# Kernel tuning notes

Hardware: AMD Instinct MI355X
Metric: run time of the kernel (lower is better)

## Reference

```python
import jax, jax.numpy as jnp
import numpy as np
import math

T, R, H, DK = 3, 4, 8, 32   # num_types, num_relations, n_heads, d_k
OUT = H * DK                # out_dim = 256
IN = 256                    # in_dim (== out_dim, required by residual)
B, N = 4, 1024              # batch, max_nodes
LN_EPS = 1e-5


def setup_inputs() -> dict:
    key = jax.random.key(0)
    ks = jax.random.split(key, 12)
    a = math.sqrt(6.0 / (2 * DK))  # xavier_uniform bound for [d_k,d_k]
    w = 0.02
    return {
        "node_features":   jax.random.normal(ks[0], (B, N, IN), jnp.float32),
        "node_types_soft": jax.random.uniform(ks[1], (B, N, T), jnp.float32),
        "adj_matrix_soft": jax.random.uniform(ks[2], (B, N, N), jnp.float32),
        "edge_types_soft": jax.random.uniform(ks[3], (B, N, N, R), jnp.float32),
        "Wq": jax.random.normal(ks[4], (T, IN, OUT), jnp.float32) * w,
        "bq": jnp.zeros((T, OUT), jnp.float32),
        "Wk": jax.random.normal(ks[5], (T, IN, OUT), jnp.float32) * w,
        "bk": jnp.zeros((T, OUT), jnp.float32),
        "Wv": jax.random.normal(ks[6], (T, IN, OUT), jnp.float32) * w,
        "bv": jnp.zeros((T, OUT), jnp.float32),
        "Wa": jax.random.normal(ks[7], (T, OUT, OUT), jnp.float32) * w,
        "ba": jnp.zeros((T, OUT), jnp.float32),
        "rel_pri": jnp.ones((R, H), jnp.float32),
        "rel_att": jax.random.uniform(ks[8], (R, H, DK, DK), jnp.float32, -a, a),
        "rel_msg": jax.random.uniform(ks[9], (R, H, DK, DK), jnp.float32, -a, a),
        "skip": jnp.ones((T,), jnp.float32),
        "ln_gamma": jnp.ones((T, OUT), jnp.float32),
        "ln_beta": jnp.zeros((T, OUT), jnp.float32),
    }


def _single(x, types, adj, erel, Wq, bq, Wk, bk, Wv, bv, Wa, ba,
            rel_pri, rel_att, rel_msg, skip, ln_gamma, ln_beta):
    # x:[N,in], types:[N,T], adj:[N,N], erel:[N,N,R]
    n = x.shape[0]
    sqrt_dk = float(np.sqrt(DK))
    # per-type projections -> [T,N,H,DK]
    Qt = (jnp.einsum('nd,tdo->tno', x, Wq) + bq[:, None, :]).reshape(T, n, H, DK)
    Kt = (jnp.einsum('nd,tdo->tno', x, Wk) + bk[:, None, :]).reshape(T, n, H, DK)
    Vt = (jnp.einsum('nd,tdo->tno', x, Wv) + bv[:, None, :]).reshape(T, n, H, DK)
    # relation-transformed K/V: [T,R,N,H,DK]
    Ksr = jnp.einsum('tnhd,rhde->trnhe', Kt, rel_att)
    Vsr = jnp.einsum('tnhd,rhde->trnhe', Vt, rel_msg)
    # soft-type mixtures (sums over target/source types factor out of the mask)
    Qbar = jnp.einsum('nt,tnhd->nhd', types, Qt)            # target mix
    Kbar = jnp.einsum('nt,trnhd->rnhd', types, Ksr)         # source mix, per relation
    # accumulated (masked, unnormalized) attention logits [N,N,H]
    res_att = jnp.zeros((n, n, H), x.dtype)
    for r in range(R):
        coef = (adj * erel[:, :, r])[:, :, None] * (rel_pri[r] / sqrt_dk)  # [N,N,H]
        res_att = res_att + coef * jnp.einsum('ihd,jhd->ijh', Qbar, Kbar[r])
    # per-target-row softmax over sources (dim j), zeroed if row-sum tiny
    row_sum = res_att.sum(axis=(1, 2))                       # [N]
    attn = jnp.where((row_sum > 1e-6)[:, None, None],
                     jax.nn.softmax(res_att, axis=1), 0.0)
    # aggregated = sum_{s,r,j} attn * masked score * V_{s,r}  (never builds [N,N,H,DK])
    agg = jnp.zeros((n, H, DK), x.dtype)
    for r in range(R):
        coef = (adj * erel[:, :, r])[:, :, None] * (rel_pri[r] / sqrt_dk)
        for s in range(T):
            score = coef * types[None, :, s, None] * jnp.einsum('ihd,jhd->ijh', Qbar, Ksr[s, r])
            agg = agg + jnp.einsum('ijh,ijh,jhd->ihd', attn, score, Vsr[s, r])
    agg = agg.reshape(n, OUT)
    # per-type output head: a_linear(gelu(agg)), gated residual, layernorm, soft-type mix
    g = jax.nn.gelu(agg, approximate=False)
    trans = jnp.einsum('no,tod->tnd', g, Wa) + ba[:, None, :]          # [T,N,OUT]
    alpha = jax.nn.sigmoid(skip)[:, None, None]
    res = trans * alpha + x[None] * (1.0 - alpha)
    mu = res.mean(axis=-1, keepdims=True)
    var = ((res - mu) ** 2).mean(axis=-1, keepdims=True)
    ln = (res - mu) / jnp.sqrt(var + LN_EPS) * ln_gamma[:, None, :] + ln_beta[:, None, :]
    return jnp.einsum('nt,tnd->nd', types, ln)


def reference(node_features, node_types_soft, adj_matrix_soft, edge_types_soft,
              Wq, bq, Wk, bk, Wv, bv, Wa, ba, rel_pri, rel_att, rel_msg,
              skip, ln_gamma, ln_beta):
    f = jax.vmap(_single, in_axes=(0, 0, 0, 0) + (None,) * 14)
    return f(node_features, node_types_soft, adj_matrix_soft, edge_types_soft,
             Wq, bq, Wk, bk, Wv, bv, Wa, ba, rel_pri, rel_att, rel_msg,
             skip, ln_gamma, ln_beta)
```

## Files before the change

### kernel.cpp

```cpp
#include <hip/hip_runtime.h>
#include <math.h>

constexpr int CB = 4, CN = 1024, CT = 3, CR = 4, CH = 8, CDK = 32, COUT = 256;

typedef __attribute__((ext_vector_type(4))) float f32x4;
typedef __attribute__((ext_vector_type(8))) short s16x8;
typedef __attribute__((ext_vector_type(2))) _Float16 f16x2;
typedef __attribute__((ext_vector_type(4))) _Float16 f16x4;
typedef __attribute__((ext_vector_type(8))) _Float16 f16x8;
typedef __attribute__((ext_vector_type(4))) unsigned short u16x4;
typedef __attribute__((ext_vector_type(8))) unsigned short u16x8;

union W4 { f16x4 v4; f16x2 v2[2]; };

__device__ inline unsigned short f2bf(float x) {
    unsigned u = __float_as_uint(x);
    unsigned r = (u + 0x7fffu + ((u >> 16) & 1u)) >> 16;
    return (unsigned short)r;
}
__device__ inline float bf2f(unsigned short b) {
    return __uint_as_float(((unsigned)b) << 16);
}
__device__ inline f16x2 pk2(float a, float b) {
    auto t = __builtin_amdgcn_cvt_pkrtz(a, b);
    f16x2 r;
    __builtin_memcpy(&r, &t, sizeof(r));
    return r;
}

__global__ __launch_bounds__(256) void prep0(
    const float* __restrict__ nf,
    unsigned short* __restrict__ Xh, unsigned short* __restrict__ Xl,
    const float* __restrict__ Wq, const float* __restrict__ Wk,
    const float* __restrict__ Wv, const float* __restrict__ Wa,
    unsigned short* __restrict__ WTh, unsigned short* __restrict__ WTl,
    const float* __restrict__ rel_msg, _Float16* __restrict__ MT,
    float* __restrict__ rs,
    const float* __restrict__ adj, const float* __restrict__ erel,
    float* __restrict__ coefT)
{
    __shared__ float smem[32 * 132];
    const int bx = blockIdx.x, tid = threadIdx.x;
    if (bx < 1024) {
        size_t idx = ((size_t)bx * 256 + tid) * 4;
        f32x4 v = *(const f32x4*)(nf + idx);
        u16x4 hv, lv;
        #pragma unroll
        for (int k = 0; k < 4; ++k) {
            unsigned short hb = f2bf(v[k]);
            hv[k] = hb; lv[k] = f2bf(v[k] - bf2f(hb));
        }
        *(u16x4*)(Xh + idx) = hv;
        *(u16x4*)(Xl + idx) = lv;
    } else if (bx < 1792) {
        int w = bx - 1024;
        int zz = w >> 6; int rem = w & 63;
        int k0 = (rem >> 3) * 32, n0 = (rem & 7) * 32;
        int t = zz % 3;
        const float* W;
        if (zz < 9) { int w3 = zz / 3; W = (w3 == 0 ? Wq : (w3 == 1 ? Wk : Wv)); }
        else W = Wa;
        W += (size_t)t * COUT * COUT;
        {
            int k = tid >> 3, n4 = (tid & 7) * 4;
            f32x4 v = *(const f32x4*)(W + (size_t)(k0 + k) * COUT + n0 + n4);
            smem[(n4 + 0) * 33 + k] = v[0]; smem[(n4 + 1) * 33 + k] = v[1];
            smem[(n4 + 2) * 33 + k] = v[2]; smem[(n4 + 3) * 33 + k] = v[3];
        }
        __syncthreads();
        int n = tid >> 3, k4 = (tid & 7) * 4;
        u16x4 hv, lv;
        #pragma unroll
        for (int j = 0; j < 4; ++j) {
            float x = smem[n * 33 + k4 + j];
            unsigned short hb = f2bf(x);
            hv[j] = hb; lv[j] = f2bf(x - bf2f(hb));
        }
        size_t off = (size_t)zz * COUT * COUT + (size_t)(n0 + n) * COUT + k0 + k4;
        *(u16x4*)(WTh + off) = hv;
        *(u16x4*)(WTl + off) = lv;
    } else if (bx < 1824) {
        int rh = bx - 1792;
        int e = tid >> 3, ep4 = (tid & 7) * 4;
        f16x4 o;
        #pragma unroll
        for (int k = 0; k < 4; ++k)
            o[k] = (_Float16)rel_msg[((size_t)rh * 32 + ep4 + k) * 32 + e];
        *(f16x4*)(MT + ((size_t)rh * 32 + e) * 32 + ep4) = o;
    } else if (bx < 1840) {
        rs[(bx - 1824) * 256 + tid] = 0.f;
    } else {
        int c = bx - 1840;
        int b = c >> 10; int rem = c & 1023;
        int i0 = (rem >> 5) * 32; int j0 = (rem & 31) * 32;
        {
            int ii = tid >> 3, jc = tid & 7;
            size_t arow = ((size_t)b * CN + i0 + ii) * CN + j0;
            f32x4 av = *(const f32x4*)(adj + arow + jc * 4);
            #pragma unroll
            for (int kk = 0; kk < 4; ++kk) {
                int j = jc * 4 + kk;
                f32x4 ev = *(const f32x4*)(erel + (arow + j) * 4);
                float a = av[kk];
                f32x4 cv;
                cv[0] = ev[0] * a; cv[1] = ev[1] * a; cv[2] = ev[2] * a; cv[3] = ev[3] * a;
                *(f32x4*)&smem[j * 132 + ii * 4] = cv;
            }
        }
        __syncthreads();
        {
            int jj = tid >> 3, ic = tid & 7;
            size_t orow = ((size_t)b * CN + j0 + jj) * CN + i0;
            #pragma unroll
            for (int kk = 0; kk < 4; ++kk)
                *(f32x4*)(coefT + (orow + ic * 4 + kk) * 4) =
                    *(const f32x4*)&smem[jj * 132 + (ic * 4 + kk) * 4];
        }
    }
}

__global__ __launch_bounds__(256) void mfma_gemm(
    int mode,
    const unsigned short* __restrict__ Ah, const unsigned short* __restrict__ Al,
    const unsigned short* __restrict__ WTh, const unsigned short* __restrict__ WTl,
    const float* __restrict__ bq, const float* __restrict__ bk,
    const float* __restrict__ bv, const float* __restrict__ ba,
    float* __restrict__ Y0, float* __restrict__ Y1, float* __restrict__ Y2)
{
    int z = blockIdx.z;
    int b, t, widx;
    const float* bias;
    float* Y;
    if (mode == 0) {
        b = z / 9; int r9 = z % 9; int w3 = r9 / 3; t = r9 % 3;
        widx = w3 * 3 + t;
        bias = (w3 == 0 ? bq : (w3 == 1 ? bk : bv)) + t * COUT;
        Y = (w3 == 0 ? Y0 : (w3 == 1 ? Y1 : Y2)) + ((size_t)b * CT + t) * CN * COUT;
    } else {
        b = z / CT; t = z % CT;
        widx = 9 + t;
        bias = ba + t * COUT;
        Y = Y0 + ((size_t)b * CT + t) * CN * COUT;
    }
    const unsigned short* Ahb = Ah + (size_t)b * CN * COUT;
    const unsigned short* Alb = Al + (size_t)b * CN * COUT;
    const unsigned short* Bhb = WTh + (size_t)widx * COUT * COUT;
    const unsigned short* Blb = WTl + (size_t)widx * COUT * COUT;

    const int M0 = blockIdx.x * 128, N0 = blockIdx.y * 128;
    __shared__ unsigned short As[2][128][40];
    __shared__ unsigned short Bs[2][128][40];
    const int tid = threadIdx.x;
    const int wave = tid >> 6, lane = tid & 63;
    const int wm = wave & 1, wn = wave >> 1;
    const int col = lane & 15, quad = lane >> 4;

    f32x4 acc[4][4];
    #pragma unroll
    for (int mt = 0; mt < 4; ++mt)
        #pragma unroll
        for (int nt = 0; nt < 4; ++nt) acc[mt][nt] = (f32x4){0.f, 0.f, 0.f, 0.f};

    for (int kt = 0; kt < COUT; kt += 32) {
        #pragma unroll
        for (int q = 0; q < 2; ++q) {
            int f = q * 256 + tid;
            int m = f >> 2, kc = (f & 3) * 8;
            *(u16x8*)&As[0][m][kc] = *(const u16x8*)(Ahb + (size_t)(M0 + m) * COUT + kt + kc);
            *(u16x8*)&As[1][m][kc] = *(const u16x8*)(Alb + (size_t)(M0 + m) * COUT + kt + kc);
            *(u16x8*)&Bs[0][m][kc] = *(const u16x8*)(Bhb + (size_t)(N0 + m) * COUT + kt + kc);
            *(u16x8*)&Bs[1][m][kc] = *(const u16x8*)(Blb + (size_t)(N0 + m) * COUT + kt + kc);
        }
        __syncthreads();
        s16x8 ah[4], al4[4], bh[4], bl4[4];
        #pragma unroll
        for (int mt = 0; mt < 4; ++mt) {
            ah[mt]  = *(const s16x8*)&As[0][wm * 64 + mt * 16 + col][quad * 8];
            al4[mt] = *(const s16x8*)&As[1][wm * 64 + mt * 16 + col][quad * 8];
        }
        #pragma unroll
        for (int nt = 0; nt < 4; ++nt) {
            bh[nt]  = *(const s16x8*)&Bs[0][wn * 64 + nt * 16 + col][quad * 8];
            bl4[nt] = *(const s16x8*)&Bs[1][wn * 64 + nt * 16 + col][quad * 8];
        }
        #pragma unroll
        for (int mt = 0; mt < 4; ++mt)
            #pragma unroll
            for (int nt = 0; nt < 4; ++nt) {
                acc[mt][nt] = __builtin_amdgcn_mfma_f32_16x16x32_bf16(al4[mt], bh[nt], acc[mt][nt], 0, 0, 0);
                acc[mt][nt] = __builtin_amdgcn_mfma_f32_16x16x32_bf16(ah[mt], bl4[nt], acc[mt][nt], 0, 0, 0);
                acc[mt][nt] = __builtin_amdgcn_mfma_f32_16x16x32_bf16(ah[mt], bh[nt], acc[mt][nt], 0, 0, 0);
            }
        __syncthreads();
    }
    float bb[4];
    #pragma unroll
    for (int nt = 0; nt < 4; ++nt) bb[nt] = bias[N0 + wn * 64 + nt * 16 + col];
    #pragma unroll
    for (int mt = 0; mt < 4; ++mt)
        #pragma unroll
        for (int nt = 0; nt < 4; ++nt) {
            int n = N0 + wn * 64 + nt * 16 + col;
            #pragma unroll
            for (int reg = 0; reg < 4; ++reg) {
                int m = M0 + wm * 64 + mt * 16 + quad * 4 + reg;
                Y[(size_t)m * COUT + n] = acc[mt][nt][reg] + bb[nt];
            }
        }
}

__global__ void mix_qbar(const float* __restrict__ Qt, const float* __restrict__ types,
                         float* __restrict__ Qbar)
{
    int idx = blockIdx.x * 256 + threadIdx.x;
    int bi = idx >> 6;
    int o4 = (idx & 63) * 4;
    int b = bi >> 10;
    const float* tp = types + (size_t)bi * CT;
    float t0 = tp[0], t1 = tp[1], t2 = tp[2];
    size_t nbase = ((size_t)b * CT) * CN * COUT + (size_t)(bi & 1023) * COUT + o4;
    float4 q0 = *(const float4*)(Qt + nbase);
    float4 q1 = *(const float4*)(Qt + nbase + (size_t)CN * COUT);
    float4 q2 = *(const float4*)(Qt + nbase + 2 * (size_t)CN * COUT);
    float4 o;
    o.x = t0 * q0.x + t1 * q1.x + t2 * q2.x;
    o.y = t0 * q0.y + t1 * q1.y + t2 * q2.y;
    o.z = t0 * q0.z + t1 * q1.z + t2 * q2.z;
    o.w = t0 * q0.w + t1 * q1.w + t2 * q2.w;
    *(float4*)(Qbar + (size_t)bi * COUT + o4) = o;
}

__global__ __launch_bounds__(256) void qr3_kernel(const float* __restrict__ Qbar,
                                                  const float* __restrict__ rel_att,
                                                  const float* __restrict__ rel_pri,
                                                  unsigned short* __restrict__ Qrhi,
                                                  unsigned short* __restrict__ Qrlo)
{
    int i0 = blockIdx.x * 8;
    int rh = blockIdx.y; int r = rh >> 3, h = rh & 7;
    int b = blockIdx.z;
    __shared__ float A_s[32][33];
    __shared__ float q_s[8][32];
    int tid = threadIdx.x;
    {
        int f = tid * 4; int d = f >> 5, e = f & 31;
        float4 v = *(const float4*)(rel_att + ((size_t)rh * 32 + d) * 32 + e);
        A_s[d][e] = v.x; A_s[d][e + 1] = v.y; A_s[d][e + 2] = v.z; A_s[d][e + 3] = v.w;
        int ii = tid >> 5, ee = tid & 31;
        q_s[ii][ee] = Qbar[((size_t)b * CN + i0 + ii) * COUT + h * CDK + ee];
    }
    __syncthreads();
    int d = tid & 31, ii = tid >> 5;
    float acc = 0.f;
    #pragma unroll 8
    for (int e = 0; e < 32; ++e) acc += A_s[d][e] * q_s[ii][e];
    const float inv_sqrt = 0.17677669529663687f;
    float v = acc * rel_pri[rh] * inv_sqrt;
    unsigned short hb = f2bf(v);
    float lo = v - bf2f(hb);
    size_t oidx = ((((size_t)b * CR + r) * CH + h) * CN + i0 + ii) * CDK + d;
    Qrhi[oidx] = hb;
    Qrlo[oidx] = f2bf(lo);
}

__global__ __launch_bounds__(256) void prep_kv(
    const float* __restrict__ Kt, const float* __restrict__ Vt,
    const float* __restrict__ types,
    unsigned short* __restrict__ Kbh, unsigned short* __restrict__ Kbl,
    unsigned short* __restrict__ Kty, _Float16* __restrict__ VT)
{
    __shared__ float tile[32][72];
    const int bx = blockIdx.x, tid = threadIdx.x;
    if (bx < 512) {
        int b = bx >> 7, jt = bx & 127;
        int j = jt * 8 + (tid >> 5);
        int c = tid & 31;
        int h = c >> 2, d0 = (c & 3) * 8;
        const float* tp = types + ((size_t)b * CN + j) * CT;
        float kb[8];
        #pragma unroll
        for (int k = 0; k < 8; ++k) kb[k] = 0.f;
        #pragma unroll
        for (int s = 0; s < 3; ++s) {
            float ty = tp[s];
            const float* src = Kt + (((size_t)(b * 3 + s)) * CN + j) * COUT + c * 8;
            f32x4 a0 = *(const f32x4*)(src);
            f32x4 a1 = *(const f32x4*)(src + 4);
            u16x8 kt8;
            #pragma unroll
            for (int k = 0; k < 4; ++k) {
                float v0 = ty * a0[k], v1 = ty * a1[k];
                kt8[k] = f2bf(v0); kt8[4 + k] = f2bf(v1);
                kb[k] += v0; kb[4 + k] += v1;
            }
            *(u16x8*)(Kty + (((size_t)(b * 3 + s) * CH + h) * CN + j) * CDK + d0) = kt8;
        }
        u16x8 hv, lv;
        #pragma unroll
        for (int k = 0; k < 8; ++k) {
            unsigned short hb = f2bf(kb[k]);
            hv[k] = hb; lv[k] = f2bf(kb[k] - bf2f(hb));
        }
        *(u16x8*)(Kbh + (((size_t)b * CH + h) * CN + j) * CDK + d0) = hv;
        *(u16x8*)(Kbl + (((size_t)b * CH + h) * CN + j) * CDK + d0) = lv;
    } else {
        int idx2 = bx - 512;
        int bs = idx2 >> 7; int rem = idx2 & 127;
        int h = rem >> 4; int j0 = (rem & 15) * 64;
        int jj = tid >> 2, e8 = (tid & 3) * 8;
        const float* src = Vt + ((size_t)bs * CN + j0 + jj) * COUT + h * CDK + e8;
        f32x4 v0 = *(const f32x4*)(src);
        f32x4 v1 = *(const f32x4*)(src + 4);
        #pragma unroll
        for (int k = 0; k < 4; ++k) { tile[e8 + k][jj] = v0[k]; tile[e8 + 4 + k][jj] = v1[k]; }
        __syncthreads();
        int e = tid >> 3, jr = (tid & 7) * 8;
        f16x8 o;
        #pragma unroll
        for (int k = 0; k < 8; ++k) o[k] = (_Float16)tile[e][jr + k];
        *(f16x8*)(VT + (((size_t)bs * CH + h) * CDK + e) * CN + j0 + jr) = o;
    }
}

__global__ __launch_bounds__(256, 3) void attn4_kernel(
    const unsigned short* __restrict__ Qrhi, const unsigned short* __restrict__ Qrlo,
    const unsigned short* __restrict__ Kbh,  const unsigned short* __restrict__ Kbl,
    const unsigned short* __restrict__ Kty,
    const _Float16* __restrict__ VT,
    const float* __restrict__ coefT,
    float* __restrict__ Upart, float* __restrict__ lbuf, float* __restrict__ rowsum)
{
    const int h = blockIdx.y;
    const int z = blockIdx.z; const int b = z >> 1, part = z & 1;
    const int tid = threadIdx.x;
    const int wave = tid >> 6, lane = tid & 63;
    const int col = lane & 15, quad = lane >> 4;
    const int i = blockIdx.x * 64 + wave * 16 + col;
    const int jbase = part * 512;

    __shared__ _Float16 vs[2][3][32][20];

    s16x8 qh[4], ql[4];
    #pragma unroll
    for (int r = 0; r < 4; ++r) {
        size_t off = ((((size_t)b * CR + r) * CH + h) * CN + i) * CDK + quad * 8;
        qh[r] = *(const s16x8*)(Qrhi + off);
        ql[r] = *(const s16x8*)(Qrlo + off);
    }

    const int e_st = tid >> 3, jc_st = tid & 7;
    size_t vtb[3];
    #pragma unroll
    for (int s = 0; s < 3; ++s)
        vtb[s] = (((size_t)(b * 3 + s) * CH + h) * CDK + e_st) * CN + jc_st * 2;

    #pragma unroll
    for (int s = 0; s < 3; ++s)
        *(unsigned*)&vs[0][s][e_st][jc_st * 2] = *(const unsigned*)(VT + vtb[s] + jbase);

    f32x4 U[4][2];
    #pragma unroll
    for (int r = 0; r < 4; ++r) { U[r][0] = (f32x4){0.f,0.f,0.f,0.f}; U[r][1] = (f32x4){0.f,0.f,0.f,0.f}; }
    float lpart = 0.f, rspart = 0.f;

    const size_t kbbase = (((size_t)b * CH + h) * CN + col) * CDK + quad * 8;
    size_t ktbase[3];
    #pragma unroll
    for (int s = 0; s < 3; ++s)
        ktbase[s] = (((size_t)(b * 3 + s) * CH + h) * CN + col) * CDK + quad * 8;
    const size_t cfrow = ((size_t)b * CN + quad * 4) * CN + i;

    s16x8 p_bh[2], p_bl[2];
    f32x4 p_cf[2][4];
    {
        const int j0 = jbase;
        p_bh[0] = *(const s16x8*)(Kbh + kbbase + (size_t)j0 * CDK);
        p_bl[0] = *(const s16x8*)(Kbl + kbbase + (size_t)j0 * CDK);
        #pragma unroll
        for (int reg = 0; reg < 4; ++reg)
            p_cf[0][reg] = *(const f32x4*)(coefT + (cfrow + (size_t)(j0 + reg) * CN) * 4);
    }
    __syncthreads();

    #pragma unroll 2
    for (int js = 0; js < 32; ++js) {
        const int cur = js & 1, nx = cur ^ 1;
        const int j0 = jbase + js * 16;
        const int buf = js & 1;
        s16x8 kt0 = *(const s16x8*)(Kty + ktbase[0] + (size_t)j0 * CDK);
        s16x8 kt1 = *(const s16x8*)(Kty + ktbase[1] + (size_t)j0 * CDK);
        s16x8 kt2 = *(const s16x8*)(Kty + ktbase[2] + (size_t)j0 * CDK);
        const int jn = jbase + ((js + 1 < 32) ? (js + 1) * 16 : js * 16);
        unsigned pf0 = *(const unsigned*)(VT + vtb[0] + jn);
        unsigned pf1 = *(const unsigned*)(VT + vtb[1] + jn);
        unsigned pf2 = *(const unsigned*)(VT + vtb[2] + jn);
        p_bh[nx] = *(const s16x8*)(Kbh + kbbase + (size_t)jn * CDK);
        p_bl[nx] = *(const s16x8*)(Kbl + kbbase + (size_t)jn * CDK);
        #pragma unroll
        for (int reg = 0; reg < 4; ++reg)
            p_cf[nx][reg] = *(const f32x4*)(coefT + (cfrow + (size_t)(jn + reg) * CN) * 4);

        f32x4 Db[4];
        #pragma unroll
        for (int r = 0; r < 4; ++r) {
            f32x4 d = {0.f, 0.f, 0.f, 0.f};
            d = __builtin_amdgcn_mfma_f32_16x16x32_bf16(p_bl[cur], qh[r], d, 0, 0, 0);
            d = __builtin_amdgcn_mfma_f32_16x16x32_bf16(p_bh[cur], ql[r], d, 0, 0, 0);
            d = __builtin_amdgcn_mfma_f32_16x16x32_bf16(p_bh[cur], qh[r], d, 0, 0, 0);
            Db[r] = d;
        }
        float P[4];
        #pragma unroll
        for (int reg = 0; reg < 4; ++reg) {
            float L = p_cf[cur][reg][0] * Db[0][reg] + p_cf[cur][reg][1] * Db[1][reg]
                    + p_cf[cur][reg][2] * Db[2][reg] + p_cf[cur][reg][3] * Db[3][reg];
            rspart += L;
            P[reg] = __expf(L);
            lpart += P[reg];
        }
        f16x2 pA[4], pB[4];
        #pragma unroll
        for (int r = 0; r < 4; ++r) {
            pA[r] = pk2(P[0] * p_cf[cur][0][r], P[1] * p_cf[cur][1][r]);
            pB[r] = pk2(P[2] * p_cf[cur][2][r], P[3] * p_cf[cur][3][r]);
        }
        #pragma unroll
        for (int s = 0; s < 3; ++s) {
            s16x8 kts = (s == 0) ? kt0 : (s == 1) ? kt1 : kt2;
            f32x4 Dp[4];
            #pragma unroll
            for (int r = 0; r < 4; ++r) {
                f32x4 d = {0.f, 0.f, 0.f, 0.f};
                Dp[r] = __builtin_amdgcn_mfma_f32_16x16x32_bf16(kts, qh[r], d, 0, 0, 0);
            }
            f16x4 v0 = *(const f16x4*)&vs[buf][s][col][quad * 4];
            f16x4 v1 = *(const f16x4*)&vs[buf][s][col + 16][quad * 4];
            #pragma unroll
            for (int r = 0; r < 4; ++r) {
                W4 w;
                w.v2[0] = pA[r] * pk2(Dp[r][0], Dp[r][1]);
                w.v2[1] = pB[r] * pk2(Dp[r][2], Dp[r][3]);
                U[r][0] = __builtin_amdgcn_mfma_f32_16x16x16f16(v0, w.v4, U[r][0], 0, 0, 0);
                U[r][1] = __builtin_amdgcn_mfma_f32_16x16x16f16(v1, w.v4, U[r][1], 0, 0, 0);
            }
        }
        *(unsigned*)&vs[buf ^ 1][0][e_st][jc_st * 2] = pf0;
        *(unsigned*)&vs[buf ^ 1][1][e_st][jc_st * 2] = pf1;
        *(unsigned*)&vs[buf ^ 1][2][e_st][jc_st * 2] = pf2;
        __syncthreads();
    }

    float l = lpart;  l += __shfl_xor(l, 16);  l += __shfl_xor(l, 32);
    float rv = rspart; rv += __shfl_xor(rv, 16); rv += __shfl_xor(rv, 32);
    if (quad == 0) {
        lbuf[(((size_t)part * CB + b) * CH + h) * CN + i] = l;
        atomicAdd(rowsum + (size_t)b * CN + i, rv);
    }
    int itile = blockIdx.x * 4 + wave;
    size_t ub = ((((size_t)(b * CH + h) * 64 + itile) * 2 + part)) * 2048;
    #pragma unroll
    for (int r = 0; r < 4; ++r)
        #pragma unroll
        for (int eh = 0; eh < 2; ++eh)
            *(f32x4*)(Upart + ub + (size_t)(r * 2 + eh) * 256 + lane * 4) = U[r][eh];
}

__global__ __launch_bounds__(256) void merge_gelu(
    const float* __restrict__ Upart, const float* __restrict__ lbuf,
    const _Float16* __restrict__ MT, const float* __restrict__ rowsum,
    unsigned short* __restrict__ Gh, unsigned short* __restrict__ Gl)
{
    const int h = blockIdx.y, b = blockIdx.z;
    const int tid = threadIdx.x;
    const int wave = tid >> 6, lane = tid & 63;
    const int col = lane & 15, quad = lane >> 4;
    const int itile = blockIdx.x * 4 + wave;
    const int i = itile * 16 + col;

    size_t ub = ((size_t)(b * CH + h) * 64 + itile) * 2 * 2048;
    f32x4 U[4][2];
    #pragma unroll
    for (int r = 0; r < 4; ++r)
        #pragma unroll
        for (int eh = 0; eh < 2; ++eh) {
            f32x4 a = *(const f32x4*)(Upart + ub + (size_t)(r * 2 + eh) * 256 + lane * 4);
            f32x4 c = *(const f32x4*)(Upart + ub + 2048 + (size_t)(r * 2 + eh) * 256 + lane * 4);
            U[r][eh] = a + c;
        }
    float l = lbuf[(((size_t)0 * CB + b) * CH + h) * CN + i]
            + lbuf[(((size_t)1 * CB + b) * CH + h) * CN + i];
    float il = 1.f / l;
    f16x4 Uh[4][2];
    #pragma unroll
    for (int r = 0; r < 4; ++r)
        #pragma unroll
        for (int eh = 0; eh < 2; ++eh) {
            Uh[r][eh][0] = (_Float16)(U[r][eh][0] * il);
            Uh[r][eh][1] = (_Float16)(U[r][eh][1] * il);
            Uh[r][eh][2] = (_Float16)(U[r][eh][2] * il);
            Uh[r][eh][3] = (_Float16)(U[r][eh][3] * il);
        }
    float rsv = rowsum[(size_t)b * CN + i];
    bool gate = rsv > 1e-6f;
    const float is2 = 0.70710678118654752f;
    #pragma unroll
    for (int eo = 0; eo < 2; ++eo) {
        f32x4 acc = {0.f, 0.f, 0.f, 0.f};
        #pragma unroll
        for (int r = 0; r < 4; ++r)
            #pragma unroll
            for (int ep = 0; ep < 2; ++ep) {
                f16x4 mt = *(const f16x4*)(MT + ((size_t)(r * 8 + h) * 32 + eo * 16 + col) * 32
                                               + ep * 16 + quad * 4);
                acc = __builtin_amdgcn_mfma_f32_16x16x16f16(mt, Uh[r][ep], acc, 0, 0, 0);
            }
        u16x4 hv, lv;
        #pragma unroll
        for (int k = 0; k < 4; ++k) {
            float x = gate ? acc[k] : 0.f;
            float g = 0.5f * x * (1.f + erff(x * is2));
            unsigned short hb = f2bf(g);
            hv[k] = hb; lv[k] = f2bf(g - bf2f(hb));
        }
        size_t off = ((size_t)b * CN + i) * COUT + h * CDK + eo * 16 + quad * 4;
        *(u16x4*)(Gh + off) = hv;
        *(u16x4*)(Gl + off) = lv;
    }
}

__global__ __launch_bounds__(256) void final_ln2(
    const float* __restrict__ trans, const float* __restrict__ x,
    const float* __restrict__ types, const float* __restrict__ skip,
    const float* __restrict__ gamma, const float* __restrict__ beta,
    float* __restrict__ out)
{
    int wave = threadIdx.x >> 6, lane = threadIdx.x & 63;
    int bi = blockIdx.x * 4 + wave;
    int b = bi >> 10, i = bi & 1023;
    f32x4 xo = *(const f32x4*)(x + (size_t)bi * COUT + lane * 4);
    f32x4 accum = {0.f, 0.f, 0.f, 0.f};
    const float* tp = types + (size_t)bi * CT;
    #pragma unroll 1
    for (int t = 0; t < CT; ++t) {
        float al = 1.f / (1.f + __expf(-skip[t]));
        f32x4 tr = *(const f32x4*)(trans + (((size_t)b * CT + t) * CN + i) * COUT + lane * 4);
        f32x4 res;
        float s = 0.f;
        #pragma unroll
        for (int k = 0; k < 4; ++k) { res[k] = tr[k] * al + xo[k] * (1.f - al); s += res[k]; }
        #pragma unroll
        for (int mk = 1; mk < 64; mk <<= 1) s += __shfl_xor(s, mk);
        float mu = s * (1.f / COUT);
        f32x4 dc; float s2 = 0.f;
        #pragma unroll
        for (int k = 0; k < 4; ++k) { dc[k] = res[k] - mu; s2 += dc[k] * dc[k]; }
        #pragma unroll
        for (int mk = 1; mk < 64; mk <<= 1) s2 += __shfl_xor(s2, mk);
        float inv = rsqrtf(s2 * (1.f / COUT) + 1e-5f);
        f32x4 g = *(const f32x4*)(gamma + (size_t)t * COUT + lane * 4);
        f32x4 be = *(const f32x4*)(beta + (size_t)t * COUT + lane * 4);
        float ty = tp[t];
        #pragma unroll
        for (int k = 0; k < 4; ++k) accum[k] += ty * (dc[k] * inv * g[k] + be[k]);
    }
    *(f32x4*)(out + (size_t)bi * COUT + lane * 4) = accum;
}

extern "C" void kernel_launch(void* const* d_in, const int* in_sizes, int n_in,
                              void* d_out, int out_size, void* d_ws, size_t ws_size,
                              hipStream_t stream)
{
    (void)in_sizes; (void)n_in; (void)out_size; (void)ws_size;
    const float* nf      = (const float*)d_in[0];
    const float* types   = (const float*)d_in[1];
    const float* adj     = (const float*)d_in[2];
    const float* erel    = (const float*)d_in[3];
    const float* Wq      = (const float*)d_in[4];
    const float* bq      = (const float*)d_in[5];
    const float* Wk      = (const float*)d_in[6];
    const float* bk      = (const float*)d_in[7];
    const float* Wv      = (const float*)d_in[8];
    const float* bv      = (const float*)d_in[9];
    const float* Wa      = (const float*)d_in[10];
    const float* ba      = (const float*)d_in[11];
    const float* rel_pri = (const float*)d_in[12];
    const float* rel_att = (const float*)d_in[13];
    const float* rel_msg = (const float*)d_in[14];
    const float* skip    = (const float*)d_in[15];
    const float* gamma   = (const float*)d_in[16];
    const float* beta    = (const float*)d_in[17];
    float* out = (float*)d_out;

    float* ws = (float*)d_ws;
    size_t o = 0;
    float* pool0 = ws + o; o += 3 * (size_t)CB * CT * CN * COUT;
    float* Qt  = pool0;
    float* Ktb = pool0 + (size_t)CB * CT * CN * COUT;
    float* Vtb = pool0 + 2 * (size_t)CB * CT * CN * COUT;
    float* Qbar = ws + o; o += (size_t)CB * CN * COUT;
    float* rsb  = ws + o; o += (size_t)CB * CN;
    float* lbufp = ws + o; o += 2 * (size_t)CB * CH * CN;
    unsigned short* Qrhi = (unsigned short*)(ws + o); o += (size_t)CB * CR * CN * COUT / 2;
    unsigned short* Qrlo = (unsigned short*)(ws + o); o += (size_t)CB * CR * CN * COUT / 2;
    unsigned short* Kbh  = (unsigned short*)(ws + o); o += (size_t)CB * CH * CN * CDK / 2;
    unsigned short* Kbl  = (unsigned short*)(ws + o); o += (size_t)CB * CH * CN * CDK / 2;
    unsigned short* Kty  = (unsigned short*)(ws + o); o += (size_t)CB * CT * CH * CN * CDK / 2;
    _Float16* VTb = (_Float16*)(ws + o);              o += (size_t)CB * CT * CH * CDK * CN / 2;
    _Float16* MTb = (_Float16*)(ws + o);              o += (size_t)CR * CH * CDK * CDK / 2;
    unsigned short* Xh = (unsigned short*)(ws + o);   o += (size_t)CB * CN * COUT / 2;
    unsigned short* Xl = (unsigned short*)(ws + o);   o += (size_t)CB * CN * COUT / 2;
    unsigned short* Gh = (unsigned short*)(ws + o);   o += (size_t)CB * CN * COUT / 2;
    unsigned short* Gl = (unsigned short*)(ws + o);   o += (size_t)CB * CN * COUT / 2;
    unsigned short* WTh = (unsigned short*)(ws + o);  o += (size_t)12 * COUT * COUT / 2;
    unsigned short* WTl = (unsigned short*)(ws + o);  o += (size_t)12 * COUT * COUT / 2;
    float* coefT = ws + o; o += (size_t)CB * CN * CN * CR;
    float* Upart  = pool0;
    float* transb = pool0 + 3 * (size_t)CB * CN * COUT;

    prep0<<<5936, 256, 0, stream>>>(nf, Xh, Xl, Wq, Wk, Wv, Wa, WTh, WTl,
                                    rel_msg, MTb, rsb, adj, erel, coefT);
    mfma_gemm<<<dim3(8, 2, CB * 9), 256, 0, stream>>>(0, Xh, Xl, WTh, WTl,
                                                      bq, bk, bv, ba, Qt, Ktb, Vtb);
    mix_qbar<<<CB * CN * COUT / 4 / 256, 256, 0, stream>>>(Qt, types, Qbar);
    qr3_kernel<<<dim3(CN / 8, CR * CH, CB), 256, 0, stream>>>(Qbar, rel_att, rel_pri, Qrhi, Qrlo);
    prep_kv<<<2048, 256, 0, stream>>>(Ktb, Vtb, types, Kbh, Kbl, Kty, VTb);
    attn4_kernel<<<dim3(16, CH, CB * 2), 256, 0, stream>>>(Qrhi, Qrlo, Kbh, Kbl, Kty, VTb, coefT,
                                                           Upart, lbufp, rsb);
    merge_gelu<<<dim3(16, CH, CB), 256, 0, stream>>>(Upart, lbufp, MTb, rsb, Gh, Gl);
    mfma_gemm<<<dim3(8, 2, CB * CT), 256, 0, stream>>>(1, Gh, Gl, WTh, WTl,
                                                       bq, bk, bv, ba, transb, transb, transb);
    final_ln2<<<CB * CN / 4, 256, 0, stream>>>(transb, nf, types, skip, gamma, beta, out);
}
```

Baseline: 374.7 us.

## Tile V layout in prep_kv so attention loads MFMA operands directly from global

prep_kv now writes V transposed into 16-column j-tiles of 512 halves, laid out so each lane's MFMA A-operand fragment is a contiguous f16x4. The attention kernel drops its shared-memory V double buffer and the per-iteration __syncthreads, and instead prefetches the fragments from global memory into registers one step ahead. This removes LDS traffic and block-wide barriers from the inner loop. In exchange it issues more global loads per lane and uses more registers for the prefetch buffers, which could lower occupancy.

New measurement: 423.6 us. +13.0%, slower.

```diff
diff --git a/kernel.cpp b/kernel.cpp
--- a/kernel.cpp
+++ b/kernel.cpp
@@ -318,11 +318,13 @@
         f16x8 o;
         #pragma unroll
         for (int k = 0; k < 8; ++k) o[k] = (_Float16)tile[e][jr + k];
-        *(f16x8*)(VT + (((size_t)bs * CH + h) * CDK + e) * CN + j0 + jr) = o;
-    }
-}
-
-__global__ __launch_bounds__(256, 3) void attn4_kernel(
+        int jg = j0 + jr;
+        int js = jg >> 4, jp = jg & 15;
+        *(f16x8*)(VT + ((size_t)(bs * CH + h) * 64 + js) * 512 + e * 16 + jp) = o;
+    }
+}
+
+__global__ __launch_bounds__(256, 3) void attn5_kernel(
     const unsigned short* __restrict__ Qrhi, const unsigned short* __restrict__ Qrlo,
     const unsigned short* __restrict__ Kbh,  const unsigned short* __restrict__ Kbl,
     const unsigned short* __restrict__ Kty,
@@ -338,8 +340,6 @@
     const int i = blockIdx.x * 64 + wave * 16 + col;
     const int jbase = part * 512;
 
-    __shared__ _Float16 vs[2][3][32][20];
-
     s16x8 qh[4], ql[4];
     #pragma unroll
     for (int r = 0; r < 4; ++r) {
@@ -348,16 +348,6 @@
         ql[r] = *(const s16x8*)(Qrlo + off);
     }
 
-    const int e_st = tid >> 3, jc_st = tid & 7;
-    size_t vtb[3];
-    #pragma unroll
-    for (int s = 0; s < 3; ++s)
-        vtb[s] = (((size_t)(b * 3 + s) * CH + h) * CDK + e_st) * CN + jc_st * 2;
-
-    #pragma unroll
-    for (int s = 0; s < 3; ++s)
-        *(unsigned*)&vs[0][s][e_st][jc_st * 2] = *(const unsigned*)(VT + vtb[s] + jbase);
-
     f32x4 U[4][2];
     #pragma unroll
     for (int r = 0; r < 4; ++r) { U[r][0] = (f32x4){0.f,0.f,0.f,0.f}; U[r][1] = (f32x4){0.f,0.f,0.f,0.f}; }
@@ -369,9 +359,14 @@
     for (int s = 0; s < 3; ++s)
         ktbase[s] = (((size_t)(b * 3 + s) * CH + h) * CN + col) * CDK + quad * 8;
     const size_t cfrow = ((size_t)b * CN + quad * 4) * CN + i;
+    size_t vb[3];
+    #pragma unroll
+    for (int s = 0; s < 3; ++s)
+        vb[s] = ((size_t)((b * 3 + s) * CH + h) * 64) * 512 + col * 16 + quad * 4;
 
     s16x8 p_bh[2], p_bl[2];
     f32x4 p_cf[2][4];
+    f16x4 p_v0[2][3], p_v1[2][3];
     {
         const int j0 = jbase;
         p_bh[0] = *(const s16x8*)(Kbh + kbbase + (size_t)j0 * CDK);
@@ -379,26 +374,33 @@
         #pragma unroll
         for (int reg = 0; reg < 4; ++reg)
             p_cf[0][reg] = *(const f32x4*)(coefT + (cfrow + (size_t)(j0 + reg) * CN) * 4);
-    }
-    __syncthreads();
+        const size_t vo = (size_t)(j0 >> 4) * 512;
+        #pragma unroll
+        for (int s = 0; s < 3; ++s) {
+            p_v0[0][s] = *(const f16x4*)(VT + vb[s] + vo);
+            p_v1[0][s] = *(const f16x4*)(VT + vb[s] + vo + 256);
+        }
+    }
 
     #pragma unroll 2
     for (int js = 0; js < 32; ++js) {
         const int cur = js & 1, nx = cur ^ 1;
         const int j0 = jbase + js * 16;
-        const int buf = js & 1;
         s16x8 kt0 = *(const s16x8*)(Kty + ktbase[0] + (size_t)j0 * CDK);
         s16x8 kt1 = *(const s16x8*)(Kty + ktbase[1] + (size_t)j0 * CDK);
         s16x8 kt2 = *(const s16x8*)(Kty + ktbase[2] + (size_t)j0 * CDK);
         const int jn = jbase + ((js + 1 < 32) ? (js + 1) * 16 : js * 16);
-        unsigned pf0 = *(const unsigned*)(VT + vtb[0] + jn);
-        unsigned pf1 = *(const unsigned*)(VT + vtb[1] + jn);
-        unsigned pf2 = *(const unsigned*)(VT + vtb[2] + jn);
         p_bh[nx] = *(const s16x8*)(Kbh + kbbase + (size_t)jn * CDK);
         p_bl[nx] = *(const s16x8*)(Kbl + kbbase + (size_t)jn * CDK);
         #pragma unroll
         for (int reg = 0; reg < 4; ++reg)
             p_cf[nx][reg] = *(const f32x4*)(coefT + (cfrow + (size_t)(jn + reg) * CN) * 4);
+        const size_t von = (size_t)(jn >> 4) * 512;
+        #pragma unroll
+        for (int s = 0; s < 3; ++s) {
+            p_v0[nx][s] = *(const f16x4*)(VT + vb[s] + von);
+            p_v1[nx][s] = *(const f16x4*)(VT + vb[s] + von + 256);
+        }
 
         f32x4 Db[4];
         #pragma unroll
@@ -433,8 +435,8 @@
                 f32x4 d = {0.f, 0.f, 0.f, 0.f};
                 Dp[r] = __builtin_amdgcn_mfma_f32_16x16x32_bf16(kts, qh[r], d, 0, 0, 0);
             }
-            f16x4 v0 = *(const f16x4*)&vs[buf][s][col][quad * 4];
-            f16x4 v1 = *(const f16x4*)&vs[buf][s][col + 16][quad * 4];
+            f16x4 v0 = p_v0[cur][s];
+            f16x4 v1 = p_v1[cur][s];
             #pragma unroll
             for (int r = 0; r < 4; ++r) {
                 W4 w;
@@ -444,10 +446,6 @@
                 U[r][1] = __builtin_amdgcn_mfma_f32_16x16x16f16(v1, w.v4, U[r][1], 0, 0, 0);
             }
         }
-        *(unsigned*)&vs[buf ^ 1][0][e_st][jc_st * 2] = pf0;
-        *(unsigned*)&vs[buf ^ 1][1][e_st][jc_st * 2] = pf1;
-        *(unsigned*)&vs[buf ^ 1][2][e_st][jc_st * 2] = pf2;
-        __syncthreads();
     }
 
     float l = lpart;  l += __shfl_xor(l, 16);  l += __shfl_xor(l, 32);
@@ -624,7 +622,7 @@
     mix_qbar<<<CB * CN * COUT / 4 / 256, 256, 0, stream>>>(Qt, types, Qbar);
     qr3_kernel<<<dim3(CN / 8, CR * CH, CB), 256, 0, stream>>>(Qbar, rel_att, rel_pri, Qrhi, Qrlo);
     prep_kv<<<2048, 256, 0, stream>>>(Ktb, Vtb, types, Kbh, Kbl, Kty, VTb);
-    attn4_kernel<<<dim3(16, CH, CB * 2), 256, 0, stream>>>(Qrhi, Qrlo, Kbh, Kbl, Kty, VTb, coefT,
+    attn5_kernel<<<dim3(16, CH, CB * 2), 256, 0, stream>>>(Qrhi, Qrlo, Kbh, Kbl, Kty, VTb, coefT,
                                                            Upart, lbufp, rsb);
     merge_gelu<<<dim3(16, CH, CB), 256, 0, stream>>>(Upart, lbufp, MTb, rsb, Gh, Gl);
     mfma_gemm<<<dim3(8, 2, CB * CT), 256, 0, stream>>>(1, Gh, Gl, WTh, WTl,
```
